# Kernel tuning notes

Measured on AMD Instinct MI355X. Metric: run time of the kernel, lower is better.

Reference implementation:

```python
import jax, jax.numpy as jnp
import numpy as np

EPS = 1e-12  # F.normalize default eps


def _wn_weight(v, g):
    # PyTorch weight_norm over dims (in, kernel) per output channel
    norm = jnp.sqrt(jnp.sum(v * v, axis=1, keepdims=True))
    return g[:, None] * v / norm


def _l2_normalize(x, axis=-1):
    n = jnp.sqrt(jnp.sum(x * x, axis=axis, keepdims=True))
    return x / jnp.maximum(n, EPS)


def setup_inputs() -> dict:
    key = jax.random.key(0)
    ks = jax.random.split(key, 8)
    B, D_IN, T = 16, 1024, 2048
    K, D_CB = 4096, 256
    s = 0.02
    return {
        "z": jax.random.normal(ks[0], (B, D_IN, T), dtype=jnp.float32),
        "in_v": jax.random.normal(ks[1], (D_CB, D_IN), dtype=jnp.float32) * s,
        "in_g": jax.random.uniform(ks[2], (D_CB,), dtype=jnp.float32, minval=0.5, maxval=1.5),
        "in_b": jax.random.normal(ks[3], (D_CB,), dtype=jnp.float32) * s,
        "out_v": jax.random.normal(ks[4], (D_IN, D_CB), dtype=jnp.float32) * s,
        "out_g": jax.random.uniform(ks[5], (D_IN,), dtype=jnp.float32, minval=0.5, maxval=1.5),
        "out_b": jax.random.normal(ks[6], (D_IN,), dtype=jnp.float32) * s,
        "codebook": jax.random.normal(ks[7], (K, D_CB), dtype=jnp.float32),
    }


def reference(z, in_v, in_g, in_b, out_v, out_g, out_b, codebook):
    B, _, T = z.shape
    # in_proj: weight-normalized 1x1 conv == per-frame matmul
    W_in = _wn_weight(in_v, in_g)            # (D_cb, D_in)
    z_i = jnp.einsum("oc,bct->bot", W_in, z) + in_b[None, :, None]  # (B, D_cb, T)

    # decode_latents: factorized, L2-normalized nearest-neighbor lookup
    enc = z_i.transpose(0, 2, 1).reshape(-1, z_i.shape[1])  # (B*T, D_cb)
    enc_n = _l2_normalize(enc)
    cb_n = _l2_normalize(codebook)
    dist = (
        jnp.sum(enc_n * enc_n, axis=1, keepdims=True)
        - 2.0 * enc_n @ cb_n.T
        + jnp.sum(cb_n * cb_n, axis=1)[None, :]
    )  # (B*T, K)
    indices = jnp.argmax(-dist, axis=1).reshape(B, T)       # (B, T)
    z_q = codebook[indices].transpose(0, 2, 1)              # (B, D_cb, T)

    # straight-through estimator
    z_q = z_i + jax.lax.stop_gradient(z_q - z_i)

    # out_proj
    W_out = _wn_weight(out_v, out_g)         # (D_in, D_cb)
    z_o = jnp.einsum("oc,bct->bot", W_out, z_q) + out_b[None, :, None]  # (B, D_in, T)
    return (z_i, z_q, z_o, indices)
```

## Files before the change

### kernel.cpp

```cpp
#include <hip/hip_runtime.h>
#include <hip/hip_bf16.h>

#define BATCH 16
#define D_IN  1024
#define T_LEN 2048
#define K_CB  4096
#define D_CB  256

#define ZI_OFF 0
#define ZQ_OFF (BATCH * D_CB * T_LEN)
#define ZO_OFF (ZQ_OFF + BATCH * D_CB * T_LEN)
#define IDX_OFF (ZO_OFF + BATCH * D_IN * T_LEN)

typedef _Float16 half8 __attribute__((ext_vector_type(8)));
typedef _Float16 h4_t  __attribute__((ext_vector_type(4)));
typedef float floatx4 __attribute__((ext_vector_type(4)));

__device__ __forceinline__ float block_sum256(float v) {
    __shared__ float sred[4];
    #pragma unroll
    for (int off = 32; off > 0; off >>= 1) v += __shfl_down(v, off, 64);
    if ((threadIdx.x & 63) == 0) sred[threadIdx.x >> 6] = v;
    __syncthreads();
    float r = sred[0] + sred[1] + sred[2] + sred[3];
    __syncthreads();
    return r;
}

__global__ __launch_bounds__(256) void wn_rows(const float* __restrict__ v,
                                               const float* __restrict__ g,
                                               float* __restrict__ W, int N) {
    int row = blockIdx.x;
    const float* src = v + (size_t)row * N;
    float ss = 0.f;
    for (int c = threadIdx.x; c < N; c += 256) { float x = src[c]; ss += x * x; }
    ss = block_sum256(ss);
    float scale = g[row] * __frsqrt_rn(ss);
    for (int c = threadIdx.x; c < N; c += 256) W[(size_t)row * N + c] = src[c] * scale;
}

__global__ __launch_bounds__(256) void cb_prep(const float* __restrict__ cb,
                                               _Float16* __restrict__ cbt) {
    int row = blockIdx.x;
    int c = threadIdx.x;
    float x = cb[(size_t)row * D_CB + c];
    float ss = block_sum256(x * x);
    float scale = 1.0f / fmaxf(sqrtf(ss), 1e-12f);
    float v = x * scale;
    _Float16 h1 = (_Float16)v;
    _Float16 h2 = (_Float16)(v - (float)h1);
    int tt = row >> 4, lo4 = row & 15;
    int ks = c >> 5, quad = (c >> 3) & 3, j = c & 7;
    size_t base = ((size_t)(tt * 16 + ks * 2)) * 512 + (quad * 16 + lo4) * 8 + j;
    cbt[base] = h1;
    cbt[base + 512] = h2;
}

template <int KDIM, int M>
__global__ __launch_bounds__(256, 2) void proj_mfma(const float* __restrict__ W,
                                                    const float* __restrict__ bias,
                                                    const float* __restrict__ Z,
                                                    float* __restrict__ Out) {
    __shared__ _Float16 A_s[2][128][40];
    __shared__ _Float16 B_s[2][128][40];

    const int tid  = threadIdx.x;
    const int wv   = tid >> 6;
    const int lane = tid & 63;
    const int lo4  = lane & 15, quad = lane >> 4;
    const int wm   = wv & 1,  wn  = wv >> 1;

    const int f0 = blockIdx.x * 128;
    const int b  = f0 >> 11;
    const int t0 = f0 & (T_LEN - 1);
    const int o0 = blockIdx.y * 128;
    const float* __restrict__ Zb = Z + (size_t)b * KDIM * T_LEN;

    const int a_g  = tid >> 5;
    const int a_tl = tid & 31;

    float  pa[4][4];
    float4 pb[4];

    floatx4 acc[4][4];
    #pragma unroll
    for (int i = 0; i < 4; i++)
        #pragma unroll
        for (int j = 0; j < 4; j++) acc[i][j] = (floatx4){0.f, 0.f, 0.f, 0.f};

    #pragma unroll
    for (int p = 0; p < 4; p++)
        #pragma unroll
        for (int j = 0; j < 4; j++)
            pa[p][j] = Zb[(size_t)(a_g * 4 + j) * T_LEN + t0 + p * 32 + a_tl];
    #pragma unroll
    for (int p = 0; p < 4; p++) {
        int idx = tid + p * 256;
        pb[p] = *(const float4*)&W[(size_t)(o0 + (idx >> 3)) * KDIM + (idx & 7) * 4];
    }

    for (int kk = 0; kk < KDIM; kk += 32) {
        #pragma unroll
        for (int p = 0; p < 4; p++) {
            int f = p * 32 + a_tl;
            h4_t h1, h2;
            #pragma unroll
            for (int j = 0; j < 4; j++) {
                float v = pa[p][j];
                _Float16 x = (_Float16)v;
                h1[j] = x;
                h2[j] = (_Float16)(v - (float)x);
            }
            *(h4_t*)&A_s[0][f][a_g * 4] = h1;
            *(h4_t*)&A_s[1][f][a_g * 4] = h2;
        }
        #pragma unroll
        for (int p = 0; p < 4; p++) {
            int idx = tid + p * 256;
            int o = idx >> 3, k4 = (idx & 7) * 4;
            h4_t h1, h2;
            #pragma unroll
            for (int j = 0; j < 4; j++) {
                float v = ((const float*)&pb[p])[j];
                _Float16 x = (_Float16)v;
                h1[j] = x;
                h2[j] = (_Float16)(v - (float)x);
            }
            *(h4_t*)&B_s[0][o][k4] = h1;
            *(h4_t*)&B_s[1][o][k4] = h2;
        }
        __syncthreads();

        if (kk + 32 < KDIM) {
            #pragma unroll
            for (int p = 0; p < 4; p++)
                #pragma unroll
                for (int j = 0; j < 4; j++)
                    pa[p][j] = Zb[(size_t)(kk + 32 + a_g * 4 + j) * T_LEN + t0 + p * 32 + a_tl];
            #pragma unroll
            for (int p = 0; p < 4; p++) {
                int idx = tid + p * 256;
                pb[p] = *(const float4*)&W[(size_t)(o0 + (idx >> 3)) * KDIM + kk + 32 + (idx & 7) * 4];
            }
        }

        half8 a1[4], a2[4], b1[4], b2[4];
        #pragma unroll
        for (int mi = 0; mi < 4; mi++) {
            a1[mi] = *(const half8*)&A_s[0][wm * 64 + mi * 16 + lo4][quad * 8];
            a2[mi] = *(const half8*)&A_s[1][wm * 64 + mi * 16 + lo4][quad * 8];
        }
        #pragma unroll
        for (int ni = 0; ni < 4; ni++) {
            b1[ni] = *(const half8*)&B_s[0][wn * 64 + ni * 16 + lo4][quad * 8];
            b2[ni] = *(const half8*)&B_s[1][wn * 64 + ni * 16 + lo4][quad * 8];
        }
        #pragma unroll
        for (int mi = 0; mi < 4; mi++)
            #pragma unroll
            for (int ni = 0; ni < 4; ni++) {
                acc[mi][ni] = __builtin_amdgcn_mfma_f32_16x16x32_f16(a1[mi], b1[ni], acc[mi][ni], 0, 0, 0);
                acc[mi][ni] = __builtin_amdgcn_mfma_f32_16x16x32_f16(a1[mi], b2[ni], acc[mi][ni], 0, 0, 0);
                acc[mi][ni] = __builtin_amdgcn_mfma_f32_16x16x32_f16(a2[mi], b1[ni], acc[mi][ni], 0, 0, 0);
            }
        __syncthreads();
    }

    #pragma unroll
    for (int ni = 0; ni < 4; ni++) {
        int o = o0 + wn * 64 + ni * 16 + lo4;
        float bv = bias[o];
        #pragma unroll
        for (int mi = 0; mi < 4; mi++) {
            int t = t0 + wm * 64 + mi * 16 + quad * 4;
            floatx4 r = acc[mi][ni];
            float4 st = make_float4(r[0] + bv, r[1] + bv, r[2] + bv, r[3] + bv);
            *(float4*)&Out[((size_t)b * M + o) * T_LEN + t] = st;
        }
    }
}

__global__ __launch_bounds__(256, 2) void vq_mfma(const float* __restrict__ z_i,
                                                  const _Float16* __restrict__ cbt,
                                                  const float* __restrict__ cb,
                                                  float* __restrict__ z_q,
                                                  float* __restrict__ idx_out) {
    __shared__ _Float16 e_s[2][32][264];
    __shared__ float red_v[4][32];
    __shared__ int   red_i[4][32];
    __shared__ int   idx_s[32];

    const int tid  = threadIdx.x;
    const int wv   = tid >> 6;
    const int lane = tid & 63;
    const int lo4  = lane & 15, quad = lane >> 4;
    const int f0 = blockIdx.x * 32;
    const int b  = f0 >> 11;
    const int t0 = f0 & (T_LEN - 1);

    for (int i = tid; i < 32 * 256; i += 256) {
        int k = i >> 5, t = i & 31;
        float v = z_i[((size_t)(b * D_CB + k)) * T_LEN + t0 + t];
        _Float16 h1 = (_Float16)v;
        _Float16 h2 = (_Float16)(v - (float)h1);
        e_s[0][t][k] = h1;
        e_s[1][t][k] = h2;
    }
    __syncthreads();

    half8 a1[2][8], a2[2][8];
    #pragma unroll
    for (int m = 0; m < 2; m++)
        #pragma unroll
        for (int ks = 0; ks < 8; ks++) {
            a1[m][ks] = *(const half8*)&e_s[0][m * 16 + lo4][ks * 32 + quad * 8];
            a2[m][ks] = *(const half8*)&e_s[1][m * 16 + lo4][ks * 32 + quad * 8];
        }

    float best_v[2][4];
    int   best_i[2][4];
    #pragma unroll
    for (int m = 0; m < 2; m++)
        #pragma unroll
        for (int r = 0; r < 4; r++) { best_v[m][r] = -3.4e38f; best_i[m][r] = 0; }

    const int tt0 = wv * 64;
    const _Float16* cb_lane = cbt + lane * 8;

    half8 b1[8], b2[8];
    #pragma unroll
    for (int ks = 0; ks < 8; ks++) {
        b1[ks] = *(const half8*)(cb_lane + (size_t)tt0 * 8192 + ks * 1024);
        b2[ks] = *(const half8*)(cb_lane + (size_t)tt0 * 8192 + ks * 1024 + 512);
    }

    for (int tt = tt0; tt < tt0 + 64; tt++) {
        floatx4 accA[2], accB[2];
        #pragma unroll
        for (int m = 0; m < 2; m++) { accA[m] = (floatx4){0.f,0.f,0.f,0.f}; accB[m] = (floatx4){0.f,0.f,0.f,0.f}; }

        const int ttn = (tt + 1 < tt0 + 64) ? tt + 1 : tt0;
        const _Float16* nb = cb_lane + (size_t)ttn * 8192;

        #pragma unroll
        for (int ks = 0; ks < 8; ks++) {
            half8 cb1 = b1[ks], cb2 = b2[ks];
            accA[0] = __builtin_amdgcn_mfma_f32_16x16x32_f16(a1[0][ks], cb1, accA[0], 0, 0, 0);
            accB[0] = __builtin_amdgcn_mfma_f32_16x16x32_f16(a1[0][ks], cb2, accB[0], 0, 0, 0);
            accA[0] = __builtin_amdgcn_mfma_f32_16x16x32_f16(a2[0][ks], cb1, accA[0], 0, 0, 0);
            accA[1] = __builtin_amdgcn_mfma_f32_16x16x32_f16(a1[1][ks], cb1, accA[1], 0, 0, 0);
            accB[1] = __builtin_amdgcn_mfma_f32_16x16x32_f16(a1[1][ks], cb2, accB[1], 0, 0, 0);
            accA[1] = __builtin_amdgcn_mfma_f32_16x16x32_f16(a2[1][ks], cb1, accA[1], 0, 0, 0);
            b1[ks] = *(const half8*)(nb + ks * 1024);
            b2[ks] = *(const half8*)(nb + ks * 1024 + 512);
        }

        const int cwi = tt * 16 + lo4;
        #pragma unroll
        for (int m = 0; m < 2; m++)
            #pragma unroll
            for (int r = 0; r < 4; r++) {
                float v = accA[m][r] + accB[m][r];
                if (v > best_v[m][r] || (v == best_v[m][r] && cwi < best_i[m][r])) {
                    best_v[m][r] = v; best_i[m][r] = cwi;
                }
            }
    }

    #pragma unroll
    for (int m = 0; m < 2; m++)
        #pragma unroll
        for (int r = 0; r < 4; r++) {
            float bv = best_v[m][r]; int bi = best_i[m][r];
            #pragma unroll
            for (int off = 8; off > 0; off >>= 1) {
                float ov = __shfl_down(bv, off, 16);
                int   oi = __shfl_down(bi, off, 16);
                if (ov > bv || (ov == bv && oi < bi)) { bv = ov; bi = oi; }
            }
            if (lo4 == 0) {
                red_v[wv][m * 16 + quad * 4 + r] = bv;
                red_i[wv][m * 16 + quad * 4 + r] = bi;
            }
        }
    __syncthreads();
    if (tid < 32) {
        float bv = red_v[0][tid]; int bi = red_i[0][tid];
        #pragma unroll
        for (int w = 1; w < 4; w++) {
            float ov = red_v[w][tid]; int oi = red_i[w][tid];
            if (ov > bv || (ov == bv && oi < bi)) { bv = ov; bi = oi; }
        }
        idx_s[tid] = bi;
        idx_out[f0 + tid] = (float)bi;
    }
    __syncthreads();

    for (int i = tid; i < 32 * 256; i += 256) {
        int k = i >> 5, t = i & 31;
        z_q[((size_t)(b * D_CB + k)) * T_LEN + t0 + t] = cb[(size_t)idx_s[t] * D_CB + k];
    }
}

extern "C" void kernel_launch(void* const* d_in, const int* in_sizes, int n_in,
                              void* d_out, int out_size, void* d_ws, size_t ws_size,
                              hipStream_t stream) {
    const float* z     = (const float*)d_in[0];
    const float* in_v  = (const float*)d_in[1];
    const float* in_g  = (const float*)d_in[2];
    const float* in_b  = (const float*)d_in[3];
    const float* out_v = (const float*)d_in[4];
    const float* out_g = (const float*)d_in[5];
    const float* out_b = (const float*)d_in[6];
    const float* cb    = (const float*)d_in[7];

    float* ws    = (float*)d_ws;
    float* W_in  = ws;
    float* W_out = ws + 262144;
    _Float16* cbt = (_Float16*)(ws + 524288);

    float* out  = (float*)d_out;
    float* z_i  = out + ZI_OFF;
    float* z_q  = out + ZQ_OFF;
    float* z_o  = out + ZO_OFF;
    float* idxf = out + IDX_OFF;

    wn_rows<<<D_CB, 256, 0, stream>>>(in_v, in_g, W_in, D_IN);
    wn_rows<<<D_IN, 256, 0, stream>>>(out_v, out_g, W_out, D_CB);
    cb_prep<<<K_CB, 256, 0, stream>>>(cb, cbt);

    proj_mfma<D_IN, D_CB><<<dim3((BATCH * T_LEN) / 128, D_CB / 128), 256, 0, stream>>>(W_in, in_b, z, z_i);

    vq_mfma<<<(BATCH * T_LEN) / 32, 256, 0, stream>>>(z_i, cbt, cb, z_q, idxf);

    proj_mfma<D_CB, D_IN><<<dim3((BATCH * T_LEN) / 128, D_IN / 128), 256, 0, stream>>>(W_out, out_b, z_q, z_o);
}
```

Baseline: 586.4 us.

## Pre-split weights into MFMA layout and widen VQ frames per block

The weight-norm kernel now writes weights already split into hi/lo fp16 pairs in the MFMA fragment layout. The projection kernels load B fragments straight from global memory instead of converting through shared memory. The VQ kernel gives each wave 32 distinct frames (128 per block), so every wave scans the full codebook instead of a quarter of it. This removes the cross-wave reduction, and waves are kept in step by a per-iteration barrier so codebook loads are shared through cache. A separate accumulator is also added to break the MFMA dependency chain, at the cost of more registers and barrier stalls.

```diff
diff --git a/kernel.cpp b/kernel.cpp
--- a/kernel.cpp
+++ b/kernel.cpp
@@ -29,14 +29,24 @@
 
 __global__ __launch_bounds__(256) void wn_rows(const float* __restrict__ v,
                                                const float* __restrict__ g,
-                                               float* __restrict__ W, int N) {
+                                               _Float16* __restrict__ wp, int N) {
     int row = blockIdx.x;
     const float* src = v + (size_t)row * N;
     float ss = 0.f;
     for (int c = threadIdx.x; c < N; c += 256) { float x = src[c]; ss += x * x; }
     ss = block_sum256(ss);
     float scale = g[row] * __frsqrt_rn(ss);
-    for (int c = threadIdx.x; c < N; c += 256) W[(size_t)row * N + c] = src[c] * scale;
+    int otile = row >> 4, lo4o = row & 15;
+    int nks = N >> 5;
+    for (int c = threadIdx.x; c < N; c += 256) {
+        float val = src[c] * scale;
+        _Float16 h1 = (_Float16)val;
+        _Float16 h2 = (_Float16)(val - (float)h1);
+        int ks = c >> 5, quad = (c >> 3) & 3, j = c & 7;
+        size_t base = ((size_t)(otile * nks + ks) * 2) * 512 + (quad * 16 + lo4o) * 8 + j;
+        wp[base] = h1;
+        wp[base + 512] = h2;
+    }
 }
 
 __global__ __launch_bounds__(256) void cb_prep(const float* __restrict__ cb,
@@ -57,12 +67,11 @@
 }
 
 template <int KDIM, int M>
-__global__ __launch_bounds__(256, 2) void proj_mfma(const float* __restrict__ W,
+__global__ __launch_bounds__(256, 2) void proj_mfma(const _Float16* __restrict__ wp,
                                                     const float* __restrict__ bias,
                                                     const float* __restrict__ Z,
                                                     float* __restrict__ Out) {
     __shared__ _Float16 A_s[2][128][40];
-    __shared__ _Float16 B_s[2][128][40];
 
     const int tid  = threadIdx.x;
     const int wv   = tid >> 6;
@@ -75,12 +84,13 @@
     const int t0 = f0 & (T_LEN - 1);
     const int o0 = blockIdx.y * 128;
     const float* __restrict__ Zb = Z + (size_t)b * KDIM * T_LEN;
+    const _Float16* __restrict__ wp_lane = wp + lane * 8;
+    const int otile_base = (o0 >> 4) + wn * 4;
 
     const int a_g  = tid >> 5;
     const int a_tl = tid & 31;
 
-    float  pa[4][4];
-    float4 pb[4];
+    float pa[4][4];
 
     floatx4 acc[4][4];
     #pragma unroll
@@ -93,11 +103,6 @@
         #pragma unroll
         for (int j = 0; j < 4; j++)
             pa[p][j] = Zb[(size_t)(a_g * 4 + j) * T_LEN + t0 + p * 32 + a_tl];
-    #pragma unroll
-    for (int p = 0; p < 4; p++) {
-        int idx = tid + p * 256;
-        pb[p] = *(const float4*)&W[(size_t)(o0 + (idx >> 3)) * KDIM + (idx & 7) * 4];
-    }
 
     for (int kk = 0; kk < KDIM; kk += 32) {
         #pragma unroll
@@ -114,21 +119,6 @@
             *(h4_t*)&A_s[0][f][a_g * 4] = h1;
             *(h4_t*)&A_s[1][f][a_g * 4] = h2;
         }
-        #pragma unroll
-        for (int p = 0; p < 4; p++) {
-            int idx = tid + p * 256;
-            int o = idx >> 3, k4 = (idx & 7) * 4;
-            h4_t h1, h2;
-            #pragma unroll
-            for (int j = 0; j < 4; j++) {
-                float v = ((const float*)&pb[p])[j];
-                _Float16 x = (_Float16)v;
-                h1[j] = x;
-                h2[j] = (_Float16)(v - (float)x);
-            }
-            *(h4_t*)&B_s[0][o][k4] = h1;
-            *(h4_t*)&B_s[1][o][k4] = h2;
-        }
         __syncthreads();
 
         if (kk + 32 < KDIM) {
@@ -137,23 +127,22 @@
                 #pragma unroll
                 for (int j = 0; j < 4; j++)
                     pa[p][j] = Zb[(size_t)(kk + 32 + a_g * 4 + j) * T_LEN + t0 + p * 32 + a_tl];
-            #pragma unroll
-            for (int p = 0; p < 4; p++) {
-                int idx = tid + p * 256;
-                pb[p] = *(const float4*)&W[(size_t)(o0 + (idx >> 3)) * KDIM + kk + 32 + (idx & 7) * 4];
-            }
-        }
-
-        half8 a1[4], a2[4], b1[4], b2[4];
+        }
+
+        const int kk32 = kk >> 5;
+        half8 b1[4], b2[4];
+        #pragma unroll
+        for (int ni = 0; ni < 4; ni++) {
+            const _Float16* src = wp_lane + ((size_t)((otile_base + ni) * (KDIM / 32) + kk32) * 2) * 512;
+            b1[ni] = *(const half8*)(src);
+            b2[ni] = *(const half8*)(src + 512);
+        }
+
+        half8 a1[4], a2[4];
         #pragma unroll
         for (int mi = 0; mi < 4; mi++) {
             a1[mi] = *(const half8*)&A_s[0][wm * 64 + mi * 16 + lo4][quad * 8];
             a2[mi] = *(const half8*)&A_s[1][wm * 64 + mi * 16 + lo4][quad * 8];
-        }
-        #pragma unroll
-        for (int ni = 0; ni < 4; ni++) {
-            b1[ni] = *(const half8*)&B_s[0][wn * 64 + ni * 16 + lo4][quad * 8];
-            b2[ni] = *(const half8*)&B_s[1][wn * 64 + ni * 16 + lo4][quad * 8];
         }
         #pragma unroll
         for (int mi = 0; mi < 4; mi++)
@@ -186,36 +175,38 @@
                                                   float* __restrict__ z_q,
                                                   float* __restrict__ idx_out) {
     __shared__ _Float16 e_s[2][32][264];
-    __shared__ float red_v[4][32];
-    __shared__ int   red_i[4][32];
-    __shared__ int   idx_s[32];
+    __shared__ int idx_s[128];
 
     const int tid  = threadIdx.x;
     const int wv   = tid >> 6;
     const int lane = tid & 63;
     const int lo4  = lane & 15, quad = lane >> 4;
-    const int f0 = blockIdx.x * 32;
+    const int f0 = blockIdx.x * 128;
     const int b  = f0 >> 11;
     const int t0 = f0 & (T_LEN - 1);
 
-    for (int i = tid; i < 32 * 256; i += 256) {
-        int k = i >> 5, t = i & 31;
-        float v = z_i[((size_t)(b * D_CB + k)) * T_LEN + t0 + t];
-        _Float16 h1 = (_Float16)v;
-        _Float16 h2 = (_Float16)(v - (float)h1);
-        e_s[0][t][k] = h1;
-        e_s[1][t][k] = h2;
-    }
-    __syncthreads();
-
     half8 a1[2][8], a2[2][8];
-    #pragma unroll
-    for (int m = 0; m < 2; m++)
-        #pragma unroll
-        for (int ks = 0; ks < 8; ks++) {
-            a1[m][ks] = *(const half8*)&e_s[0][m * 16 + lo4][ks * 32 + quad * 8];
-            a2[m][ks] = *(const half8*)&e_s[1][m * 16 + lo4][ks * 32 + quad * 8];
-        }
+    for (int ph = 0; ph < 4; ph++) {
+        for (int i = tid; i < 32 * 256; i += 256) {
+            int k = i >> 5, t = i & 31;
+            float v = z_i[((size_t)(b * D_CB + k)) * T_LEN + t0 + ph * 32 + t];
+            _Float16 h1 = (_Float16)v;
+            _Float16 h2 = (_Float16)(v - (float)h1);
+            e_s[0][t][k] = h1;
+            e_s[1][t][k] = h2;
+        }
+        __syncthreads();
+        if (wv == ph) {
+            #pragma unroll
+            for (int m = 0; m < 2; m++)
+                #pragma unroll
+                for (int ks = 0; ks < 8; ks++) {
+                    a1[m][ks] = *(const half8*)&e_s[0][m * 16 + lo4][ks * 32 + quad * 8];
+                    a2[m][ks] = *(const half8*)&e_s[1][m * 16 + lo4][ks * 32 + quad * 8];
+                }
+        }
+        __syncthreads();
+    }
 
     float best_v[2][4];
     int   best_i[2][4];
@@ -224,22 +215,26 @@
         #pragma unroll
         for (int r = 0; r < 4; r++) { best_v[m][r] = -3.4e38f; best_i[m][r] = 0; }
 
-    const int tt0 = wv * 64;
     const _Float16* cb_lane = cbt + lane * 8;
 
     half8 b1[8], b2[8];
     #pragma unroll
     for (int ks = 0; ks < 8; ks++) {
-        b1[ks] = *(const half8*)(cb_lane + (size_t)tt0 * 8192 + ks * 1024);
-        b2[ks] = *(const half8*)(cb_lane + (size_t)tt0 * 8192 + ks * 1024 + 512);
-    }
-
-    for (int tt = tt0; tt < tt0 + 64; tt++) {
-        floatx4 accA[2], accB[2];
-        #pragma unroll
-        for (int m = 0; m < 2; m++) { accA[m] = (floatx4){0.f,0.f,0.f,0.f}; accB[m] = (floatx4){0.f,0.f,0.f,0.f}; }
-
-        const int ttn = (tt + 1 < tt0 + 64) ? tt + 1 : tt0;
+        b1[ks] = *(const half8*)(cb_lane + ks * 1024);
+        b2[ks] = *(const half8*)(cb_lane + ks * 1024 + 512);
+    }
+
+    for (int tt = 0; tt < 256; tt++) {
+        __builtin_amdgcn_s_barrier();
+        floatx4 accA[2], accB[2], accC[2];
+        #pragma unroll
+        for (int m = 0; m < 2; m++) {
+            accA[m] = (floatx4){0.f,0.f,0.f,0.f};
+            accB[m] = (floatx4){0.f,0.f,0.f,0.f};
+            accC[m] = (floatx4){0.f,0.f,0.f,0.f};
+        }
+
+        const int ttn = (tt + 1 < 256) ? tt + 1 : 0;
         const _Float16* nb = cb_lane + (size_t)ttn * 8192;
 
         #pragma unroll
@@ -247,10 +242,10 @@
             half8 cb1 = b1[ks], cb2 = b2[ks];
             accA[0] = __builtin_amdgcn_mfma_f32_16x16x32_f16(a1[0][ks], cb1, accA[0], 0, 0, 0);
             accB[0] = __builtin_amdgcn_mfma_f32_16x16x32_f16(a1[0][ks], cb2, accB[0], 0, 0, 0);
-            accA[0] = __builtin_amdgcn_mfma_f32_16x16x32_f16(a2[0][ks], cb1, accA[0], 0, 0, 0);
+            accC[0] = __builtin_amdgcn_mfma_f32_16x16x32_f16(a2[0][ks], cb1, accC[0], 0, 0, 0);
             accA[1] = __builtin_amdgcn_mfma_f32_16x16x32_f16(a1[1][ks], cb1, accA[1], 0, 0, 0);
             accB[1] = __builtin_amdgcn_mfma_f32_16x16x32_f16(a1[1][ks], cb2, accB[1], 0, 0, 0);
-            accA[1] = __builtin_amdgcn_mfma_f32_16x16x32_f16(a2[1][ks], cb1, accA[1], 0, 0, 0);
+            accC[1] = __builtin_amdgcn_mfma_f32_16x16x32_f16(a2[1][ks], cb1, accC[1], 0, 0, 0);
             b1[ks] = *(const half8*)(nb + ks * 1024);
             b2[ks] = *(const half8*)(nb + ks * 1024 + 512);
         }
@@ -260,7 +255,7 @@
         for (int m = 0; m < 2; m++)
             #pragma unroll
             for (int r = 0; r < 4; r++) {
-                float v = accA[m][r] + accB[m][r];
+                float v = accA[m][r] + accB[m][r] + accC[m][r];
                 if (v > best_v[m][r] || (v == best_v[m][r] && cwi < best_i[m][r])) {
                     best_v[m][r] = v; best_i[m][r] = cwi;
                 }
@@ -279,25 +274,15 @@
                 if (ov > bv || (ov == bv && oi < bi)) { bv = ov; bi = oi; }
             }
             if (lo4 == 0) {
-                red_v[wv][m * 16 + quad * 4 + r] = bv;
-                red_i[wv][m * 16 + quad * 4 + r] = bi;
+                int fr = wv * 32 + m * 16 + quad * 4 + r;
+                idx_s[fr] = bi;
+                idx_out[f0 + fr] = (float)bi;
             }
         }
     __syncthreads();
-    if (tid < 32) {
-        float bv = red_v[0][tid]; int bi = red_i[0][tid];
-        #pragma unroll
-        for (int w = 1; w < 4; w++) {
-            float ov = red_v[w][tid]; int oi = red_i[w][tid];
-            if (ov > bv || (ov == bv && oi < bi)) { bv = ov; bi = oi; }
-        }
-        idx_s[tid] = bi;
-        idx_out[f0 + tid] = (float)bi;
-    }
-    __syncthreads();
-
-    for (int i = tid; i < 32 * 256; i += 256) {
-        int k = i >> 5, t = i & 31;
+
+    for (int i = tid; i < 128 * 256; i += 256) {
+        int k = i >> 7, t = i & 127;
         z_q[((size_t)(b * D_CB + k)) * T_LEN + t0 + t] = cb[(size_t)idx_s[t] * D_CB + k];
     }
 }
@@ -314,10 +299,10 @@
     const float* out_b = (const float*)d_in[6];
     const float* cb    = (const float*)d_in[7];
 
-    float* ws    = (float*)d_ws;
-    float* W_in  = ws;
-    float* W_out = ws + 262144;
-    _Float16* cbt = (_Float16*)(ws + 524288);
+    float* ws = (float*)d_ws;
+    _Float16* wp_in  = (_Float16*)ws;
+    _Float16* wp_out = (_Float16*)(ws + 262144);
+    _Float16* cbt    = (_Float16*)(ws + 524288);
 
     float* out  = (float*)d_out;
     float* z_i  = out + ZI_OFF;
@@ -325,13 +310,13 @@
     float* z_o  = out + ZO_OFF;
     float* idxf = out + IDX_OFF;
 
-    wn_rows<<<D_CB, 256, 0, stream>>>(in_v, in_g, W_in, D_IN);
-    wn_rows<<<D_IN, 256, 0, stream>>>(out_v, out_g, W_out, D_CB);
+    wn_rows<<<D_CB, 256, 0, stream>>>(in_v, in_g, wp_in, D_IN);
+    wn_rows<<<D_IN, 256, 0, stream>>>(out_v, out_g, wp_out, D_CB);
     cb_prep<<<K_CB, 256, 0, stream>>>(cb, cbt);
 
-    proj_mfma<D_IN, D_CB><<<dim3((BATCH * T_LEN) / 128, D_CB / 128), 256, 0, stream>>>(W_in, in_b, z, z_i);
-
-    vq_mfma<<<(BATCH * T_LEN) / 32, 256, 0, stream>>>(z_i, cbt, cb, z_q, idxf);
-
-    proj_mfma<D_CB, D_IN><<<dim3((BATCH * T_LEN) / 128, D_IN / 128), 256, 0, stream>>>(W_out, out_b, z_q, z_o);
-}
+    proj_mfma<D_IN, D_CB><<<dim3((BATCH * T_LEN) / 128, D_CB / 128), 256, 0, stream>>>(wp_in, in_b, z, z_i);
+
+    vq_mfma<<<(BATCH * T_LEN) / 128, 256, 0, stream>>>(z_i, cbt, cb, z_q, idxf);
+
+    proj_mfma<D_CB, D_IN><<<dim3((BATCH * T_LEN) / 128, D_IN / 128), 256, 0, stream>>>(wp_out, out_b, z_q, z_o);
+}
```

Measured after the change: 682.8 us. 1.16x slower.
